# Optimization experiments

Measured on AMD Instinct MI355X. Metric: run time of the kernel, lower is better.

Reference implementation:

```python
import jax, jax.numpy as jnp
import numpy as np

GROUP_SIZE = 128
EQN = "btd,kdf->btkf"  # x:[B,T,D] @ w:[K,D,F] -> [B,T,K,F]


def setup_inputs() -> dict:
    key = jax.random.key(0)
    k1, k2, k3, k4 = jax.random.split(key, 4)
    B, T, D = 4, 2048, 4096
    K, F = 2, 8192
    G = D // GROUP_SIZE  # 32 quantization groups along D
    x = jax.random.normal(k1, (B, T, D), dtype=jnp.float32)
    qweight = jax.random.randint(k2, (K, D, F), 0, 16, dtype=jnp.int32)  # uint4 values
    qzeros = jax.random.randint(k3, (K, G, F), 0, 16, dtype=jnp.int32)   # uint4 zero points
    scales = jax.random.uniform(k4, (K, G, F), dtype=jnp.float32) * 0.02
    return {"x": x, "qweight": qweight, "qzeros": qzeros, "scales": scales}


def dequantize(imatrix, scales, zeros, group_size, axis_to_repeat):
    rs = jnp.repeat(scales, group_size, axis=axis_to_repeat)
    rz = jnp.repeat(zeros, group_size, axis=axis_to_repeat)
    return (imatrix.astype(rs.dtype) - rz.astype(rs.dtype)) * rs


def reference(x, qweight, qzeros, scales):
    # dequantize int4 weights along axis 1 (hidden/contraction dim), then einsum
    w = dequantize(qweight, scales, qzeros, GROUP_SIZE, axis_to_repeat=1)  # [K,D,F] fp32
    w = w.astype(x.dtype)
    return jnp.einsum(EQN, x, w)  # [B,T,K,F]
```

## Files before the change

kernel.cpp:

```cpp
#include <hip/hip_runtime.h>
#include <hip/hip_bf16.h>
#include <stdint.h>


typedef __attribute__((ext_vector_type(8))) short bf16x8;
typedef __attribute__((ext_vector_type(4))) float f32x4;

static constexpr int Dd = 4096, Ff = 8192;
static constexpr int M = 8192, NTOT = 16384;
static constexpr int NKT = Dd / 64;
static constexpr int NMB = M / 256;
static constexpr int NNB = NTOT / 256;

__device__ __forceinline__ short f2bf(float f) {
    __hip_bfloat16 h = __float2bfloat16(f);
    return *reinterpret_cast<short*>(&h);
}

__global__ __launch_bounds__(256) void xcvt(const float* __restrict__ x,
                                            char* __restrict__ Xw) {
    const int bid = blockIdx.x;
    const int h = bid >> 6, kt = bid & 63;
    const int t = threadIdx.x;
    const int r = t >> 1, seg = t & 1;
    const float* src = x + ((size_t)(h * 128 + r)) * Dd + kt * 64 + seg * 32;
    char* panel = Xw + ((size_t)bid << 14);
    #pragma unroll
    for (int jj = 0; jj < 4; ++jj) {
        float4 v0 = *reinterpret_cast<const float4*>(src + jj * 8);
        float4 v1 = *reinterpret_cast<const float4*>(src + jj * 8 + 4);
        union { short s[8]; bf16x8 v; } u;
        u.s[0] = f2bf(v0.x); u.s[1] = f2bf(v0.y); u.s[2] = f2bf(v0.z); u.s[3] = f2bf(v0.w);
        u.s[4] = f2bf(v1.x); u.s[5] = f2bf(v1.y); u.s[6] = f2bf(v1.z); u.s[7] = f2bf(v1.w);
        const int cb = seg * 4 + jj;
        const int g = r * 8 + (cb ^ (r & 7));
        *reinterpret_cast<bf16x8*>(panel + g * 16) = u.v;
    }
}

__global__ __launch_bounds__(256) void wdq(const int* __restrict__ qw,
                                           const int* __restrict__ qz,
                                           const float* __restrict__ sc,
                                           char* __restrict__ Ww) {
    const int bid = blockIdx.x;
    const int fh = bid >> 6, kt = bid & 63;
    const int t = threadIdx.x;
    const int r = t & 127, dh = t >> 7;
    const int n = fh * 128 + r;
    const int k = n >> 13, f = n & 8191;
    const int g = kt >> 1;
    const int   zv = qz[((size_t)k * 32 + g) * Ff + f];
    const float sv = sc[((size_t)k * 32 + g) * Ff + f];
    const int* qp = qw + ((size_t)(k * Dd + kt * 64 + dh * 32)) * Ff + f;
    char* panel = Ww + ((size_t)bid << 14);
    #pragma unroll
    for (int jj = 0; jj < 4; ++jj) {
        union { short s[8]; bf16x8 v; } u;
        #pragma unroll
        for (int e = 0; e < 8; ++e) {
            int q = qp[(size_t)(jj * 8 + e) * Ff];
            u.s[e] = f2bf((float)(q - zv) * sv);
        }
        const int cb = dh * 4 + jj;
        const int gi = r * 8 + (cb ^ (r & 7));
        *reinterpret_cast<bf16x8*>(panel + gi * 16) = u.v;
    }
}

#define APAN(HALF, KT) (Xw + (((size_t)(bm2 + (HALF)) * 64 + (KT)) << 14))
#define BPAN(HALF, KT) (Ww + (((size_t)(bn2 + (HALF)) * 64 + (KT)) << 14))

#define STAGE(GP, LP) do {                                                         \
    const char* _g = (GP) + woff16;                                                \
    char* _l = (LP) + woffu;                                                       \
    __builtin_amdgcn_global_load_lds(                                              \
        (const __attribute__((address_space(1))) void*)(_g),                       \
        (__attribute__((address_space(3))) void*)(_l), 16, 0, 0);                  \
    __builtin_amdgcn_global_load_lds(                                              \
        (const __attribute__((address_space(1))) void*)(_g + 8192),                \
        (__attribute__((address_space(3))) void*)(_l + 8192), 16, 0, 0);           \
} while (0)

#define RDF(BASE, R, CB) \
    (*reinterpret_cast<const bf16x8*>((BASE) + ((((R) << 7) + (CB)) ^ (((R) & 7) << 4))))

#define PHASE(LA, LB, H, KK, LOADB, STG, WAITQ) do {                               \
    if (LOADB) {                                                                   \
        _Pragma("unroll")                                                          \
        for (int ni = 0; ni < 4; ++ni)                                             \
            bb[ni] = RDF((LB) + bpan, brow + ni * 16, (KK) * 2 + lhi16);           \
    }                                                                              \
    _Pragma("unroll")                                                              \
    for (int j = 0; j < 4; ++j)                                                    \
        af[j] = RDF((LA) + apan, ((H) * 4 + j) * 16 + l15, (KK) * 2 + lhi16);      \
    STG;                                                                           \
    __builtin_amdgcn_sched_barrier(0);                                             \
    __builtin_amdgcn_s_barrier();                                                  \
    asm volatile("s_waitcnt lgkmcnt(0)" ::: "memory");                             \
    __builtin_amdgcn_sched_barrier(0);                                             \
    __builtin_amdgcn_s_setprio(1);                                                 \
    _Pragma("unroll")                                                              \
    for (int j = 0; j < 4; ++j)                                                    \
        _Pragma("unroll")                                                          \
        for (int ni = 0; ni < 4; ++ni)                                             \
            acc[(H) * 4 + j][ni] = __builtin_amdgcn_mfma_f32_16x16x32_bf16(        \
                af[j], bb[ni], acc[(H) * 4 + j][ni], 0, 0, 0);                     \
    __builtin_amdgcn_s_setprio(0);                                                 \
    WAITQ;                                                                         \
    __builtin_amdgcn_sched_barrier(0);                                             \
    __builtin_amdgcn_s_barrier();                                                  \
} while (0)

__global__ __launch_bounds__(512, 2) void gemm256(const char* __restrict__ Xw,
                                                  const char* __restrict__ Ww,
                                                  float* __restrict__ out) {
    __shared__ char lds[131072];
    char* lA0 = lds;
    char* lB0 = lds + 32768;
    char* lA1 = lds + 65536;
    char* lB1 = lds + 98304;

    const int t = threadIdx.x;
    const int wave = t >> 6, lane = t & 63;
    const int wm = wave >> 2, wn = wave & 3;
    const int l15 = lane & 15, lhi16 = (lane >> 4) * 16;

    const int xcd = blockIdx.x & 7;
    const int c   = blockIdx.x >> 3;
    const int bn  = xcd * 8 + (c >> 5);
    const int bm  = c & 31;
    const int bm2 = bm * 2, bn2 = bn * 2;

    const int woff16 = wave * 1024 + lane * 16;
    const int woffu  = wave * 1024;
    const int apan = wm * 16384;
    const int bpan = (wn >> 1) * 16384;
    const int brow = (wn & 1) * 64 + l15;

    bf16x8 af[4], bb[4];
    f32x4 acc[8][4] = {};

    STAGE(APAN(0, 0), lA0);
    STAGE(APAN(1, 0), lA0 + 16384);
    STAGE(BPAN(0, 0), lB0);
    STAGE(BPAN(1, 0), lB0 + 16384);
    STAGE(BPAN(0, 1), lB1);
    asm volatile("s_waitcnt vmcnt(2)" ::: "memory");
    __builtin_amdgcn_sched_barrier(0);
    __builtin_amdgcn_s_barrier();

    for (int i = 0; i < 32; ++i) {
        const int kt0 = 2 * i;
        const bool nl = (i < 31);
        PHASE(lA0, lB0, 0, 0,  1, { STAGE(BPAN(1, kt0 + 1), lB1 + 16384); }, );
        PHASE(lA0, lB0, 1, 0,  0, { STAGE(APAN(0, kt0 + 1), lA1); }, );
        PHASE(lA0, lB0, 0, 32, 1, { STAGE(APAN(1, kt0 + 1), lA1 + 16384); }, );
        PHASE(lA0, lB0, 1, 32, 0, { if (nl) STAGE(BPAN(0, kt0 + 2), lB0); },
              { if (nl) asm volatile("s_waitcnt vmcnt(2)" ::: "memory");
                else    asm volatile("s_waitcnt vmcnt(0)" ::: "memory"); });
        PHASE(lA1, lB1, 0, 0,  1, { if (nl) STAGE(BPAN(1, kt0 + 2), lB0 + 16384); }, );
        PHASE(lA1, lB1, 1, 0,  0, { if (nl) STAGE(APAN(0, kt0 + 2), lA0); }, );
        PHASE(lA1, lB1, 0, 32, 1, { if (nl) STAGE(APAN(1, kt0 + 2), lA0 + 16384); }, );
        PHASE(lA1, lB1, 1, 32, 0, { if (nl) STAGE(BPAN(0, kt0 + 3), lB1); },
              { if (nl) asm volatile("s_waitcnt vmcnt(2)" ::: "memory");
                else    asm volatile("s_waitcnt vmcnt(0)" ::: "memory"); });
    }

    const int gr0 = bm * 256 + wm * 128 + (lhi16 >> 2);
    const int gc0 = bn * 256 + wn * 64 + l15;
    #pragma unroll
    for (int mi = 0; mi < 8; ++mi)
        #pragma unroll
        for (int ni = 0; ni < 4; ++ni)
            #pragma unroll
            for (int rr = 0; rr < 4; ++rr)
                out[(size_t)(gr0 + mi * 16 + rr) * NTOT + gc0 + ni * 16] =
                    acc[mi][ni][rr];
}

#define LDP 72
__global__ __launch_bounds__(256) void int4_gemm(
    const float* __restrict__ x, const int* __restrict__ qw,
    const int* __restrict__ qz, const float* __restrict__ sc,
    float* __restrict__ out)
{
    __shared__ short As[128][LDP];
    __shared__ short Bs[128][LDP];
    const int t = threadIdx.x;
    int gid = (blockIdx.x & 7) * 1024 + (blockIdx.x >> 3);
    const int bm = gid & 63;
    const int bnq = gid >> 6;
    const int kse = bnq >> 6;
    const int f0  = (bnq & 63) * 128;
    const int m0  = bm * 128;
    const int wave = t >> 6, lane = t & 63;
    const int wm = wave >> 1, wn = wave & 1;
    const int l15 = lane & 15, lhi = lane >> 4;
    const int am = t >> 4, ad = (t & 15) * 4;
    const int bf = t & 127, bd = (t >> 7) * 4;
    const int*   qwk = qw + (size_t)kse * Dd * Ff;
    const int*   qzk = qz + (size_t)kse * 32 * Ff;
    const float* sck = sc + (size_t)kse * 32 * Ff;
    f32x4 acc[4][4] = {};
    for (int d0 = 0; d0 < Dd; d0 += 64) {
        __syncthreads();
        #pragma unroll
        for (int p = 0; p < 8; ++p) {
            int m = p * 16 + am;
            const float4 v = *reinterpret_cast<const float4*>(
                &x[(size_t)(m0 + m) * Dd + d0 + ad]);
            short4 wv;
            wv.x = f2bf(v.x); wv.y = f2bf(v.y); wv.z = f2bf(v.z); wv.w = f2bf(v.w);
            *reinterpret_cast<short4*>(&As[m][ad]) = wv;
        }
        {
            const int g = d0 >> 7;
            const int   zv = qzk[g * Ff + f0 + bf];
            const float sv = sck[g * Ff + f0 + bf];
            #pragma unroll
            for (int p = 0; p < 8; ++p) {
                int dl = p * 8 + bd;
                const int* qp = qwk + (size_t)(d0 + dl) * Ff + f0 + bf;
                short4 wv;
                wv.x = f2bf((float)(qp[0]      - zv) * sv);
                wv.y = f2bf((float)(qp[Ff]     - zv) * sv);
                wv.z = f2bf((float)(qp[2 * Ff] - zv) * sv);
                wv.w = f2bf((float)(qp[3 * Ff] - zv) * sv);
                *reinterpret_cast<short4*>(&Bs[bf][dl]) = wv;
            }
        }
        __syncthreads();
        #pragma unroll
        for (int kk = 0; kk < 64; kk += 32) {
            bf16x8 a2[4], b2[4];
            #pragma unroll
            for (int i = 0; i < 4; ++i)
                a2[i] = *reinterpret_cast<const bf16x8*>(&As[wm * 64 + i * 16 + l15][kk + lhi * 8]);
            #pragma unroll
            for (int i = 0; i < 4; ++i)
                b2[i] = *reinterpret_cast<const bf16x8*>(&Bs[wn * 64 + i * 16 + l15][kk + lhi * 8]);
            #pragma unroll
            for (int mi = 0; mi < 4; ++mi)
                #pragma unroll
                for (int ni = 0; ni < 4; ++ni)
                    acc[mi][ni] = __builtin_amdgcn_mfma_f32_16x16x32_bf16(
                        a2[mi], b2[ni], acc[mi][ni], 0, 0, 0);
        }
    }
    const int crow0 = m0 + wm * 64 + lhi * 4;
    const int ccol0 = bnq * 128 + wn * 64 + l15;
    #pragma unroll
    for (int mi = 0; mi < 4; ++mi)
        #pragma unroll
        for (int ni = 0; ni < 4; ++ni)
            #pragma unroll
            for (int r = 0; r < 4; ++r)
                out[(size_t)(crow0 + mi * 16 + r) * NTOT + ccol0 + ni * 16] =
                    acc[mi][ni][r];
}

extern "C" void kernel_launch(void* const* d_in, const int* in_sizes, int n_in,
                              void* d_out, int out_size, void* d_ws, size_t ws_size,
                              hipStream_t stream) {
    const float* x  = (const float*)d_in[0];
    const int*   qw = (const int*)d_in[1];
    const int*   qz = (const int*)d_in[2];
    const float* sc = (const float*)d_in[3];
    float*       out = (float*)d_out;

    const size_t xw_bytes = (size_t)(M / 128) * NKT * 16384;
    const size_t ww_bytes = (size_t)(NTOT / 128) * NKT * 16384;

    if (ws_size >= xw_bytes + ww_bytes) {
        char* Xw = (char*)d_ws;
        char* Ww = Xw + xw_bytes;
        hipLaunchKernelGGL(xcvt, dim3((M / 128) * NKT), dim3(256), 0, stream, x, Xw);
        hipLaunchKernelGGL(wdq, dim3((NTOT / 128) * NKT), dim3(256), 0, stream,
                           qw, qz, sc, Ww);
        hipLaunchKernelGGL(gemm256, dim3(NMB * NNB), dim3(512), 0, stream,
                           Xw, Ww, out);
    } else {
        hipLaunchKernelGGL(int4_gemm, dim3(8192), dim3(256), 0, stream,
                           x, qw, qz, sc, out);
    }
}
```

Before: 1.152 ms.

## Double-buffer MFMA fragments in registers to overlap LDS reads with MFMAs

```diff
diff --git a/kernel.cpp b/kernel.cpp
--- a/kernel.cpp
+++ b/kernel.cpp
@@ -84,19 +84,19 @@
 #define RDF(BASE, R, CB) \
     (*reinterpret_cast<const bf16x8*>((BASE) + ((((R) << 7) + (CB)) ^ (((R) & 7) << 4))))
 
-#define PHASE(LA, LB, H, KK, LOADB, STG, WAITQ) do {                               \
-    if (LOADB) {                                                                   \
-        _Pragma("unroll")                                                          \
-        for (int ni = 0; ni < 4; ++ni)                                             \
-            bb[ni] = RDF((LB) + bpan, brow + ni * 16, (KK) * 2 + lhi16);           \
-    }                                                                              \
+#define RDA(DST, LA, H, KK) do {                                                   \
     _Pragma("unroll")                                                              \
     for (int j = 0; j < 4; ++j)                                                    \
-        af[j] = RDF((LA) + apan, ((H) * 4 + j) * 16 + l15, (KK) * 2 + lhi16);      \
-    STG;                                                                           \
-    __builtin_amdgcn_sched_barrier(0);                                             \
-    __builtin_amdgcn_s_barrier();                                                  \
-    asm volatile("s_waitcnt lgkmcnt(0)" ::: "memory");                             \
+        DST[j] = RDF((LA) + apan, ((H) * 4 + j) * 16 + l15, (KK) * 2 + lhi16);     \
+} while (0)
+
+#define RDB(DST, LB, KK) do {                                                      \
+    _Pragma("unroll")                                                              \
+    for (int ni = 0; ni < 4; ++ni)                                                 \
+        DST[ni] = RDF((LB) + bpan, brow + ni * 16, (KK) * 2 + lhi16);              \
+} while (0)
+
+#define MM(H, AF, BB) do {                                                         \
     __builtin_amdgcn_sched_barrier(0);                                             \
     __builtin_amdgcn_s_setprio(1);                                                 \
     _Pragma("unroll")                                                              \
@@ -104,9 +104,12 @@
         _Pragma("unroll")                                                          \
         for (int ni = 0; ni < 4; ++ni)                                             \
             acc[(H) * 4 + j][ni] = __builtin_amdgcn_mfma_f32_16x16x32_bf16(        \
-                af[j], bb[ni], acc[(H) * 4 + j][ni], 0, 0, 0);                     \
+                AF[j], BB[ni], acc[(H) * 4 + j][ni], 0, 0, 0);                     \
     __builtin_amdgcn_s_setprio(0);                                                 \
-    WAITQ;                                                                         \
+    __builtin_amdgcn_sched_barrier(0);                                             \
+} while (0)
+
+#define BAR() do {                                                                 \
     __builtin_amdgcn_sched_barrier(0);                                             \
     __builtin_amdgcn_s_barrier();                                                  \
 } while (0)
@@ -137,7 +140,7 @@
     const int bpan = (wn >> 1) * 16384;
     const int brow = (wn & 1) * 64 + l15;
 
-    bf16x8 af[4], bb[4];
+    bf16x8 af0[4], af1[4], bb0[4], bb1[4];
     f32x4 acc[8][4] = {};
 
     STAGE(APAN(0, 0), lA0);
@@ -146,24 +149,57 @@
     STAGE(BPAN(1, 0), lB0 + 16384);
     STAGE(BPAN(0, 1), lB1);
     asm volatile("s_waitcnt vmcnt(2)" ::: "memory");
-    __builtin_amdgcn_sched_barrier(0);
-    __builtin_amdgcn_s_barrier();
+    BAR();
+    RDB(bb0, lB0, 0);
+    RDA(af0, lA0, 0, 0);
 
     for (int i = 0; i < 32; ++i) {
         const int kt0 = 2 * i;
         const bool nl = (i < 31);
-        PHASE(lA0, lB0, 0, 0,  1, { STAGE(BPAN(1, kt0 + 1), lB1 + 16384); }, );
-        PHASE(lA0, lB0, 1, 0,  0, { STAGE(APAN(0, kt0 + 1), lA1); }, );
-        PHASE(lA0, lB0, 0, 32, 1, { STAGE(APAN(1, kt0 + 1), lA1 + 16384); }, );
-        PHASE(lA0, lB0, 1, 32, 0, { if (nl) STAGE(BPAN(0, kt0 + 2), lB0); },
-              { if (nl) asm volatile("s_waitcnt vmcnt(2)" ::: "memory");
-                else    asm volatile("s_waitcnt vmcnt(0)" ::: "memory"); });
-        PHASE(lA1, lB1, 0, 0,  1, { if (nl) STAGE(BPAN(1, kt0 + 2), lB0 + 16384); }, );
-        PHASE(lA1, lB1, 1, 0,  0, { if (nl) STAGE(APAN(0, kt0 + 2), lA0); }, );
-        PHASE(lA1, lB1, 0, 32, 1, { if (nl) STAGE(APAN(1, kt0 + 2), lA0 + 16384); }, );
-        PHASE(lA1, lB1, 1, 32, 0, { if (nl) STAGE(BPAN(0, kt0 + 3), lB1); },
-              { if (nl) asm volatile("s_waitcnt vmcnt(2)" ::: "memory");
-                else    asm volatile("s_waitcnt vmcnt(0)" ::: "memory"); });
+        STAGE(BPAN(1, kt0 + 1), lB1 + 16384);
+        BAR();
+        RDA(af1, lA0, 1, 0);
+        MM(0, af0, bb0);
+        STAGE(APAN(0, kt0 + 1), lA1);
+        BAR();
+        RDB(bb1, lB0, 32);
+        RDA(af0, lA0, 0, 32);
+        MM(1, af1, bb0);
+        STAGE(APAN(1, kt0 + 1), lA1 + 16384);
+        BAR();
+        RDA(af1, lA0, 1, 32);
+        MM(0, af0, bb1);
+        if (nl) {
+            STAGE(BPAN(0, kt0 + 2), lB0);
+            asm volatile("s_waitcnt vmcnt(2)" ::: "memory");
+        } else {
+            asm volatile("s_waitcnt vmcnt(0)" ::: "memory");
+        }
+        BAR();
+        RDB(bb0, lB1, 0);
+        RDA(af0, lA1, 0, 0);
+        MM(1, af1, bb1);
+        if (nl) STAGE(BPAN(1, kt0 + 2), lB0 + 16384);
+        BAR();
+        RDA(af1, lA1, 1, 0);
+        MM(0, af0, bb0);
+        if (nl) STAGE(APAN(0, kt0 + 2), lA0);
+        BAR();
+        RDB(bb1, lB1, 32);
+        RDA(af0, lA1, 0, 32);
+        MM(1, af1, bb0);
+        if (nl) STAGE(APAN(1, kt0 + 2), lA0 + 16384);
+        BAR();
+        RDA(af1, lA1, 1, 32);
+        MM(0, af0, bb1);
+        if (nl) {
+            STAGE(BPAN(0, kt0 + 3), lB1);
+            asm volatile("s_waitcnt vmcnt(2)" ::: "memory");
+        }
+        BAR();
+        RDB(bb0, lB0, 0);
+        RDA(af0, lA0, 0, 0);
+        MM(1, af1, bb1);
     }
 
     const int gr0 = bm * 256 + wm * 128 + (lhi16 >> 2);
```

After: 1.500 ms. +30.3%, slower.

## Restructure GEMM main loop into per-tile double-buffered schedule with fewer barriers

Applied to the files above, without the earlier changes.

```diff
diff --git a/kernel.cpp b/kernel.cpp
--- a/kernel.cpp
+++ b/kernel.cpp
@@ -84,19 +84,19 @@
 #define RDF(BASE, R, CB) \
     (*reinterpret_cast<const bf16x8*>((BASE) + ((((R) << 7) + (CB)) ^ (((R) & 7) << 4))))
 
-#define PHASE(LA, LB, H, KK, LOADB, STG, WAITQ) do {                               \
-    if (LOADB) {                                                                   \
-        _Pragma("unroll")                                                          \
-        for (int ni = 0; ni < 4; ++ni)                                             \
-            bb[ni] = RDF((LB) + bpan, brow + ni * 16, (KK) * 2 + lhi16);           \
-    }                                                                              \
+#define RDA(DST, LA, H, KK) do {                                                   \
     _Pragma("unroll")                                                              \
     for (int j = 0; j < 4; ++j)                                                    \
-        af[j] = RDF((LA) + apan, ((H) * 4 + j) * 16 + l15, (KK) * 2 + lhi16);      \
-    STG;                                                                           \
-    __builtin_amdgcn_sched_barrier(0);                                             \
-    __builtin_amdgcn_s_barrier();                                                  \
-    asm volatile("s_waitcnt lgkmcnt(0)" ::: "memory");                             \
+        DST[j] = RDF((LA) + apan, ((H) * 4 + j) * 16 + l15, (KK) * 2 + lhi16);     \
+} while (0)
+
+#define RDB(DST, LB, KK) do {                                                      \
+    _Pragma("unroll")                                                              \
+    for (int ni = 0; ni < 4; ++ni)                                                 \
+        DST[ni] = RDF((LB) + bpan, brow + ni * 16, (KK) * 2 + lhi16);              \
+} while (0)
+
+#define MM(H, AF, BB) do {                                                         \
     __builtin_amdgcn_sched_barrier(0);                                             \
     __builtin_amdgcn_s_setprio(1);                                                 \
     _Pragma("unroll")                                                              \
@@ -104,9 +104,30 @@
         _Pragma("unroll")                                                          \
         for (int ni = 0; ni < 4; ++ni)                                             \
             acc[(H) * 4 + j][ni] = __builtin_amdgcn_mfma_f32_16x16x32_bf16(        \
-                af[j], bb[ni], acc[(H) * 4 + j][ni], 0, 0, 0);                     \
+                AF[j], BB[ni], acc[(H) * 4 + j][ni], 0, 0, 0);                     \
     __builtin_amdgcn_s_setprio(0);                                                 \
-    WAITQ;                                                                         \
+    __builtin_amdgcn_sched_barrier(0);                                             \
+} while (0)
+
+#define TILE(LA, LB, LAN, LBN, KTN, DOST) do {                                     \
+    RDB(bb0, LB, 0);                                                               \
+    RDA(afa, LA, 0, 0);                                                            \
+    RDA(afb, LA, 1, 0);                                                            \
+    RDB(bb1, LB, 32);                                                              \
+    RDA(afc, LA, 0, 32);                                                           \
+    if (DOST) {                                                                    \
+        STAGE(APAN(0, KTN), LAN);                                                  \
+        STAGE(APAN(1, KTN), LAN + 16384);                                          \
+        STAGE(BPAN(0, KTN), LBN);                                                  \
+        STAGE(BPAN(1, KTN), LBN + 16384);                                          \
+    }                                                                              \
+    __builtin_amdgcn_sched_barrier(0);                                             \
+    MM(0, afa, bb0);                                                               \
+    RDA(afd, LA, 1, 32);                                                           \
+    MM(1, afb, bb0);                                                               \
+    MM(0, afc, bb1);                                                               \
+    MM(1, afd, bb1);                                                               \
+    asm volatile("s_waitcnt vmcnt(0)" ::: "memory");                               \
     __builtin_amdgcn_sched_barrier(0);                                             \
     __builtin_amdgcn_s_barrier();                                                  \
 } while (0)
@@ -137,33 +158,21 @@
     const int bpan = (wn >> 1) * 16384;
     const int brow = (wn & 1) * 64 + l15;
 
-    bf16x8 af[4], bb[4];
+    bf16x8 afa[4], afb[4], afc[4], afd[4], bb0[4], bb1[4];
     f32x4 acc[8][4] = {};
 
     STAGE(APAN(0, 0), lA0);
     STAGE(APAN(1, 0), lA0 + 16384);
     STAGE(BPAN(0, 0), lB0);
     STAGE(BPAN(1, 0), lB0 + 16384);
-    STAGE(BPAN(0, 1), lB1);
-    asm volatile("s_waitcnt vmcnt(2)" ::: "memory");
+    asm volatile("s_waitcnt vmcnt(0)" ::: "memory");
     __builtin_amdgcn_sched_barrier(0);
     __builtin_amdgcn_s_barrier();
 
     for (int i = 0; i < 32; ++i) {
-        const int kt0 = 2 * i;
-        const bool nl = (i < 31);
-        PHASE(lA0, lB0, 0, 0,  1, { STAGE(BPAN(1, kt0 + 1), lB1 + 16384); }, );
-        PHASE(lA0, lB0, 1, 0,  0, { STAGE(APAN(0, kt0 + 1), lA1); }, );
-        PHASE(lA0, lB0, 0, 32, 1, { STAGE(APAN(1, kt0 + 1), lA1 + 16384); }, );
-        PHASE(lA0, lB0, 1, 32, 0, { if (nl) STAGE(BPAN(0, kt0 + 2), lB0); },
-              { if (nl) asm volatile("s_waitcnt vmcnt(2)" ::: "memory");
-                else    asm volatile("s_waitcnt vmcnt(0)" ::: "memory"); });
-        PHASE(lA1, lB1, 0, 0,  1, { if (nl) STAGE(BPAN(1, kt0 + 2), lB0 + 16384); }, );
-        PHASE(lA1, lB1, 1, 0,  0, { if (nl) STAGE(APAN(0, kt0 + 2), lA0); }, );
-        PHASE(lA1, lB1, 0, 32, 1, { if (nl) STAGE(APAN(1, kt0 + 2), lA0 + 16384); }, );
-        PHASE(lA1, lB1, 1, 32, 0, { if (nl) STAGE(BPAN(0, kt0 + 3), lB1); },
-              { if (nl) asm volatile("s_waitcnt vmcnt(2)" ::: "memory");
-                else    asm volatile("s_waitcnt vmcnt(0)" ::: "memory"); });
+        const int kt = 2 * i;
+        TILE(lA0, lB0, lA1, lB1, kt + 1, true);
+        TILE(lA1, lB1, lA0, lB0, kt + 2, (i < 31));
     }
 
     const int gr0 = bm * 256 + wm * 128 + (lhi16 >> 2);
```

Measured after the change: 1.476 ms. +28.1%, slower.
